# Kernel optimization log

Measured on AMD Instinct MI355X. Metric: run time of the kernel, lower is better.

## Reference

```python
import jax, jax.numpy as jnp
import numpy as np

N_NODES = 40000
N_EDGES = 640000
N_GRAPHS = 64
D_IN = 128
HID = 200
OUT = 2


def _lin(key, fin, fout):
    # torch nn.Linear-style init: U(-1/sqrt(fin), 1/sqrt(fin))
    kw, kb = jax.random.split(key)
    s = 1.0 / np.sqrt(fin)
    W = jax.random.uniform(kw, (fin, fout), jnp.float32, -s, s)
    b = jax.random.uniform(kb, (fout,), jnp.float32, -s, s)
    return W, b


def setup_inputs() -> dict:
    key = jax.random.key(0)
    ks = jax.random.split(key, 10)
    x = jax.random.normal(ks[0], (N_NODES, D_IN), jnp.float32)
    edge_index = jax.random.randint(ks[1], (2, N_EDGES), 0, N_NODES, jnp.int32)
    batch = jnp.sort(jax.random.randint(ks[2], (N_NODES,), 0, N_GRAPHS, jnp.int32))
    W1, b1 = _lin(ks[3], D_IN, HID)
    W2, b2 = _lin(ks[4], HID, HID)
    W3, b3 = _lin(ks[5], HID, HID)
    Wg, bg = _lin(ks[6], HID, HID)
    Wc1, bc1 = _lin(ks[7], HID, HID // 2)
    Wc2, bc2 = _lin(ks[8], HID // 2, OUT)
    return {"x": x, "edge_index": edge_index, "batch": batch,
            "W1": W1, "b1": b1, "W2": W2, "b2": b2, "W3": W3, "b3": b3,
            "Wg": Wg, "bg": bg, "Wc1": Wc1, "bc1": bc1, "Wc2": Wc2, "bc2": bc2}


def reference(x, edge_index, batch, W1, b1, W2, b2, W3, b3, Wg, bg, Wc1, bc1, Wc2, bc2):
    n = x.shape[0]
    # GCNConv with self-loops + symmetric normalization (PyG defaults)
    loop = jnp.arange(n, dtype=edge_index.dtype)
    src = jnp.concatenate([edge_index[0], loop])  # [E+N]
    dst = jnp.concatenate([edge_index[1], loop])
    deg = jax.ops.segment_sum(jnp.ones(src.shape, x.dtype), dst, num_segments=n)
    dinv = jax.lax.rsqrt(jnp.maximum(deg, 1.0))  # deg >= 1 with self-loops
    norm = (dinv[src] * dinv[dst])[:, None]      # [E+N, 1]

    def gcn(h, W, b):
        m = (h @ W)[src] * norm                  # gather + scale per edge
        return jax.ops.segment_sum(m, dst, num_segments=n) + b

    h = jax.nn.relu(gcn(x, W1, b1))
    h = jax.nn.relu(gcn(h, W2, b2))
    h = jax.nn.relu(gcn(h, W3, b3))

    gate = jax.nn.sigmoid(h @ Wg + bg)
    hg = h * gate

    # global_mean_pool over batch assignment
    sums = jax.ops.segment_sum(hg, batch, num_segments=N_GRAPHS)
    cnt = jax.ops.segment_sum(jnp.ones((n,), x.dtype), batch, num_segments=N_GRAPHS)
    pooled = sums / jnp.maximum(cnt, 1.0)[:, None]

    # classifier (dropout is identity in eval)
    hidden = jax.nn.relu(pooled @ Wc1 + bc1)
    logits = hidden @ Wc2 + bc2                  # [N_GRAPHS, 2]
    return logits
```

## Files before the change

### kernel.cpp

```cpp
#include <hip/hip_runtime.h>

#define NG 64
#define HIDW 200
#define DIN 128
#define KPAD 224
#define POOL_NC 8

typedef _Float16 half4_t __attribute__((ext_vector_type(4)));
typedef _Float16 half8_t __attribute__((ext_vector_type(8)));
typedef float floatx4 __attribute__((ext_vector_type(4)));


__global__ void build_kernel(const int* __restrict__ dst, int* __restrict__ counts,
                             const int* __restrict__ batch, int* __restrict__ gs,
                             int E, int n) {
  int i = blockIdx.x * 256 + threadIdx.x;
  if (i < E) atomicAdd(&counts[dst[i]], 1);
  if (i < n) {
    int b = batch[i];
    if (i == 0) {
      for (int g = 0; g <= b; ++g) gs[g] = 0;
    } else {
      int bp = batch[i - 1];
      for (int g = bp + 1; g <= b; ++g) gs[g] = i;
    }
    if (i == n - 1) {
      for (int g = b + 1; g <= NG; ++g) gs[g] = n;
    }
  }
}


__global__ __launch_bounds__(256) void scan1_kernel(const int* __restrict__ counts,
                                                    int* __restrict__ blocksum,
                                                    float* __restrict__ dinv, int n) {
  __shared__ int s[256];
  int tid = threadIdx.x;
  int i = blockIdx.x * 256 + tid;
  int c = (i < n) ? counts[i] : 0;
  if (i < n) dinv[i] = rsqrtf((float)(c + 1));
  s[tid] = c;
  __syncthreads();
#pragma unroll
  for (int off = 128; off > 0; off >>= 1) {
    if (tid < off) s[tid] += s[tid + off];
    __syncthreads();
  }
  if (tid == 0) blocksum[blockIdx.x] = s[0];
}

__global__ __launch_bounds__(1024) void scan2_kernel(int* __restrict__ blocksum, int nb) {
  __shared__ int s[1024];
  int tid = threadIdx.x;
  int v = (tid < nb) ? blocksum[tid] : 0;
  s[tid] = v;
  __syncthreads();
  for (int off = 1; off < 1024; off <<= 1) {
    int t = (tid >= off) ? s[tid - off] : 0;
    __syncthreads();
    s[tid] += t;
    __syncthreads();
  }
  if (tid < nb) blocksum[tid] = s[tid] - v;
}

__global__ __launch_bounds__(256) void scan3_kernel(const int* __restrict__ counts,
                                                    const int* __restrict__ blocksum,
                                                    int* __restrict__ row_ptr, int n) {
  __shared__ int s[256];
  int tid = threadIdx.x;
  int i = blockIdx.x * 256 + tid;
  int c = (i < n) ? counts[i] : 0;
  s[tid] = c;
  __syncthreads();
  for (int off = 1; off < 256; off <<= 1) {
    int t = (tid >= off) ? s[tid - off] : 0;
    __syncthreads();
    s[tid] += t;
    __syncthreads();
  }
  int base = blocksum[blockIdx.x];
  if (i < n) row_ptr[i] = base + s[tid] - c;
  if (i == n - 1) row_ptr[n] = base + s[tid];
}

__global__ void fill_kernel(const int* __restrict__ src, const int* __restrict__ dst,
                            const int* __restrict__ row_ptr, int* __restrict__ fill,
                            int* __restrict__ csr_src, int E) {
  int e = blockIdx.x * 256 + threadIdx.x;
  if (e >= E) return;
  int d = dst[e];
  int pos = row_ptr[d] + atomicAdd(&fill[d], 1);
  csr_src[pos] = src[e];
}


__global__ void wprep_kernel(const float* __restrict__ W1, const float* __restrict__ W2,
                             const float* __restrict__ W3, const float* __restrict__ Wg,
                             _Float16* __restrict__ o1, _Float16* __restrict__ o2,
                             _Float16* __restrict__ o3, _Float16* __restrict__ og) {
  int wsel = blockIdx.y;
  const float* W = (wsel == 0) ? W1 : (wsel == 1) ? W2 : (wsel == 2) ? W3 : Wg;
  _Float16* WT = (wsel == 0) ? o1 : (wsel == 1) ? o2 : (wsel == 2) ? o3 : og;
  int K  = (wsel == 0) ? DIN : HIDW;
  int KP = (wsel == 0) ? DIN : KPAD;
  int idx = blockIdx.x * 256 + threadIdx.x;
  if (idx >= 256 * KP) return;
  int col = idx / KP, k = idx % KP;
  float v = (col < HIDW && k < K) ? W[(long)k * HIDW + col] : 0.f;
  WT[idx] = (_Float16)v;
}


__global__ void cvt_kernel(const float* __restrict__ x, const float* __restrict__ dinv,
                           _Float16* __restrict__ g0, int n) {
  int t = blockIdx.x * 256 + threadIdx.x;
  if (t >= n * 32) return;
  int node = t >> 5, q = t & 31;
  float di = dinv[node];
  float4 v = *(const float4*)&x[(long)node * 128 + q * 4];
  half4_t r = {(_Float16)(di * v.x), (_Float16)(di * v.y),
               (_Float16)(di * v.z), (_Float16)(di * v.w)};
  ((half4_t*)g0)[(long)node * 32 + q] = r;
}


template <int C>
__global__ __launch_bounds__(256) void agg_kernel(const _Float16* __restrict__ g,
                                                  const int* __restrict__ row_ptr,
                                                  const int* __restrict__ csr_src,
                                                  const float* __restrict__ dinv,
                                                  _Float16* __restrict__ out, int n) {
  int node = blockIdx.x * 4 + (threadIdx.x >> 6);
  int lane = threadIdx.x & 63;
  if (node >= n || lane >= C) return;
  const half4_t* __restrict__ hp = (const half4_t*)g;
  int e0 = row_ptr[node], e1 = row_ptr[node + 1];
  half4_t self = hp[(long)node * C + lane];
  float ax = (float)self.x, ay = (float)self.y;
  float az = (float)self.z, aw = (float)self.w;

  int e = e0;
  for (; e + 16 <= e1; e += 16) {
    int sI[16];
#pragma unroll
    for (int j = 0; j < 16; ++j) sI[j] = csr_src[e + j];
    half4_t vv[16];
#pragma unroll
    for (int j = 0; j < 16; ++j) vv[j] = hp[(long)sI[j] * C + lane];
#pragma unroll
    for (int j = 0; j < 16; ++j) {
      ax += (float)vv[j].x; ay += (float)vv[j].y;
      az += (float)vv[j].z; aw += (float)vv[j].w;
    }
  }
  if (e + 8 <= e1) {
    int sI[8];
#pragma unroll
    for (int j = 0; j < 8; ++j) sI[j] = csr_src[e + j];
    half4_t vv[8];
#pragma unroll
    for (int j = 0; j < 8; ++j) vv[j] = hp[(long)sI[j] * C + lane];
#pragma unroll
    for (int j = 0; j < 8; ++j) {
      ax += (float)vv[j].x; ay += (float)vv[j].y;
      az += (float)vv[j].z; aw += (float)vv[j].w;
    }
    e += 8;
  }
  if (e + 4 <= e1) {
    int sI[4];
#pragma unroll
    for (int j = 0; j < 4; ++j) sI[j] = csr_src[e + j];
    half4_t vv[4];
#pragma unroll
    for (int j = 0; j < 4; ++j) vv[j] = hp[(long)sI[j] * C + lane];
#pragma unroll
    for (int j = 0; j < 4; ++j) {
      ax += (float)vv[j].x; ay += (float)vv[j].y;
      az += (float)vv[j].z; aw += (float)vv[j].w;
    }
    e += 4;
  }
  for (; e < e1; ++e) {
    int s = csr_src[e];
    half4_t v = hp[(long)s * C + lane];
    ax += (float)v.x; ay += (float)v.y; az += (float)v.z; aw += (float)v.w;
  }
  float di = dinv[node];
  half4_t r = {(_Float16)(di * ax), (_Float16)(di * ay),
               (_Float16)(di * az), (_Float16)(di * aw)};
  ((half4_t*)out)[(long)node * C + lane] = r;
}


template <int KP, int MODE, int DSCALE>
__global__ __launch_bounds__(256, 2) void mgemm_kernel(const _Float16* __restrict__ A,
                                                       const _Float16* __restrict__ WT,
                                                       const float* __restrict__ bias,
                                                       const float* __restrict__ dinv,
                                                       _Float16* __restrict__ out, int N) {
  constexpr int LDK = KP + 8;
  __shared__ _Float16 Bs[64][LDK];
  int tid = threadIdx.x;
  int b = blockIdx.x;
  int strip = (b >> 3) & 3;
  int rg = (b & 7) + 8 * (b >> 5);
  int col0 = strip * 64;

  {
    int c = tid >> 2;
    int ks = (tid & 3) * (KP / 4);
    const _Float16* gw = WT + (long)(col0 + c) * KP + ks;
#pragma unroll
    for (int j = 0; j < KP / 32; ++j)
      *(half8_t*)&Bs[c][ks + j * 8] = *(const half8_t*)(gw + j * 8);
  }
  __syncthreads();

  int lane = tid & 63;
  int wid = tid >> 6;
  int row0 = rg * 256 + wid * 64;
  if (row0 >= N) return;
  int l15 = lane & 15;
  int lq = lane >> 4;

  const _Float16* __restrict__ pa = A + (long)(row0 + l15) * KP + lq * 8;

  floatx4 acc[4][4];
#pragma unroll
  for (int i = 0; i < 4; ++i)
#pragma unroll
    for (int j = 0; j < 4; ++j) acc[i][j] = (floatx4){0.f, 0.f, 0.f, 0.f};

#pragma unroll
  for (int k0 = 0; k0 < KP; k0 += 32) {
    half8_t a[4];
#pragma unroll
    for (int rf = 0; rf < 4; ++rf)
      a[rf] = *(const half8_t*)(pa + (long)rf * 16 * KP + k0);
#pragma unroll
    for (int cf = 0; cf < 4; ++cf) {
      half8_t bv = *(const half8_t*)&Bs[cf * 16 + l15][k0 + lq * 8];
#pragma unroll
      for (int rf = 0; rf < 4; ++rf)
        acc[rf][cf] = __builtin_amdgcn_mfma_f32_16x16x32_f16(a[rf], bv, acc[rf][cf], 0, 0, 0);
    }
  }

#pragma unroll
  for (int cf = 0; cf < 4; ++cf) {
    int col = col0 + cf * 16 + l15;
    if (col >= KPAD) continue;
    float bs = (col < HIDW) ? bias[col] : 0.f;
#pragma unroll
    for (int rf = 0; rf < 4; ++rf) {
      int rbase = row0 + rf * 16 + lq * 4;
#pragma unroll
      for (int j = 0; j < 4; ++j) {
        int row = rbase + j;
        float v = acc[rf][cf][j] + bs;
        if (MODE == 1) v = fmaxf(v, 0.f);
        if (MODE == 2) {
          float hv = (float)A[(long)row * KP + col];
          v = hv * (1.f / (1.f + __expf(-v)));
        }
        if (DSCALE) v *= dinv[row];
        if (col >= HIDW) v = 0.f;
        out[(long)row * KPAD + col] = (_Float16)v;
      }
    }
  }
}


__global__ __launch_bounds__(256) void pool_partial_kernel(const _Float16* __restrict__ gated,
                                                           const int* __restrict__ gs,
                                                           float* __restrict__ partial, int n) {
  int g = blockIdx.x;
  int c = blockIdx.y;
  int f = threadIdx.x;
  int s = gs[g], e = gs[g + 1];
  int len = e - s;
  int chunk = (len + POOL_NC - 1) / POOL_NC;
  int i0 = s + c * chunk;
  int i1 = i0 + chunk; if (i1 > e) i1 = e;
  if (f < HIDW) {
    float acc = 0.f;
    for (int i = i0; i < i1; ++i) acc += (float)gated[(long)i * KPAD + f];
    partial[(g * POOL_NC + c) * HIDW + f] = acc;
  }
}


__global__ void classifier_kernel(const float* __restrict__ partial,
                                  const int* __restrict__ gs,
                                  const float* __restrict__ Wc1, const float* __restrict__ bc1,
                                  const float* __restrict__ Wc2, const float* __restrict__ bc2,
                                  float* __restrict__ out) {
  int g = blockIdx.x;
  int tid = threadIdx.x;
  __shared__ float pg[HIDW];
  __shared__ float hid[100];
  if (tid < HIDW) {
    float acc = 0.f;
#pragma unroll
    for (int c = 0; c < POOL_NC; ++c) acc += partial[(g * POOL_NC + c) * HIDW + tid];
    float cnt = fmaxf((float)(gs[g + 1] - gs[g]), 1.f);
    pg[tid] = acc / cnt;
  }
  __syncthreads();
  if (tid < 100) {
    float a = bc1[tid];
    for (int k = 0; k < HIDW; ++k) a = fmaf(pg[k], Wc1[k * 100 + tid], a);
    hid[tid] = fmaxf(a, 0.f);
  }
  __syncthreads();
  if (tid < 2) {
    float a = bc2[tid];
    for (int k = 0; k < 100; ++k) a = fmaf(hid[k], Wc2[k * 2 + tid], a);
    out[g * 2 + tid] = a;
  }
}


extern "C" void kernel_launch(void* const* d_in, const int* in_sizes, int n_in,
                              void* d_out, int out_size, void* d_ws, size_t ws_size,
                              hipStream_t stream) {
  const float* x    = (const float*)d_in[0];
  const int*   ei   = (const int*)d_in[1];
  const int*   batch= (const int*)d_in[2];
  const float* W1 = (const float*)d_in[3];  const float* b1 = (const float*)d_in[4];
  const float* W2 = (const float*)d_in[5];  const float* b2 = (const float*)d_in[6];
  const float* W3 = (const float*)d_in[7];  const float* b3 = (const float*)d_in[8];
  const float* Wg = (const float*)d_in[9];  const float* bg = (const float*)d_in[10];
  const float* Wc1= (const float*)d_in[11]; const float* bc1= (const float*)d_in[12];
  const float* Wc2= (const float*)d_in[13]; const float* bc2= (const float*)d_in[14];
  float* out = (float*)d_out;

  const int n = in_sizes[0] / DIN;
  const int E = in_sizes[1] / 2;
  const int* src = ei;
  const int* dst = ei + E;
  const int nb256 = (n + 255) / 256;

  int* counts   = (int*)d_ws;
  int* fill     = counts + n;
  int* row_ptr  = fill + n;
  int* gs       = row_ptr + (n + 4);
  int* blocksum = gs + 68;
  float* dinv   = (float*)(blocksum + 1024);
  int* csr_src  = (int*)(dinv + n);
  float* partial= (float*)(csr_src + E);
  _Float16* wt1 = (_Float16*)(partial + NG * POOL_NC * HIDW);
  _Float16* wt2 = wt1 + 256 * 128;
  _Float16* wt3 = wt2 + 256 * KPAD;
  _Float16* wtg = wt3 + 256 * KPAD;
  _Float16* xh   = wtg + 256 * KPAD;
  _Float16* bufA = xh + (long)n * DIN;
  _Float16* bufB = bufA + (long)n * KPAD;

  hipMemsetAsync(counts, 0, (size_t)2 * n * sizeof(int), stream);

  dim3 wgrid((256 * KPAD + 255) / 256, 4);
  wprep_kernel<<<wgrid, 256, 0, stream>>>(W1, W2, W3, Wg, wt1, wt2, wt3, wtg);

  int eb = (E + 255) / 256;
  build_kernel<<<eb, 256, 0, stream>>>(dst, counts, batch, gs, E, n);
  scan1_kernel<<<nb256, 256, 0, stream>>>(counts, blocksum, dinv, n);
  cvt_kernel<<<(n * 32 + 255) / 256, 256, 0, stream>>>(x, dinv, xh, n);
  scan2_kernel<<<1, 1024, 0, stream>>>(blocksum, nb256);
  scan3_kernel<<<nb256, 256, 0, stream>>>(counts, blocksum, row_ptr, n);
  fill_kernel<<<eb, 256, 0, stream>>>(src, dst, row_ptr, fill, csr_src, E);

  int ab = (n + 3) / 4;
  int gb = ((nb256 + 7) / 8) * 8 * 4;

  agg_kernel<32><<<ab, 256, 0, stream>>>(xh, row_ptr, csr_src, dinv, bufA, n);
  mgemm_kernel<DIN, 1, 1><<<gb, 256, 0, stream>>>(bufA, wt1, b1, dinv, bufB, n);
  agg_kernel<56><<<ab, 256, 0, stream>>>(bufB, row_ptr, csr_src, dinv, bufA, n);
  mgemm_kernel<KPAD, 1, 1><<<gb, 256, 0, stream>>>(bufA, wt2, b2, dinv, bufB, n);
  agg_kernel<56><<<ab, 256, 0, stream>>>(bufB, row_ptr, csr_src, dinv, bufA, n);
  mgemm_kernel<KPAD, 1, 0><<<gb, 256, 0, stream>>>(bufA, wt3, b3, dinv, bufB, n);
  mgemm_kernel<KPAD, 2, 0><<<gb, 256, 0, stream>>>(bufB, wtg, bg, dinv, bufA, n);
  dim3 pgrid(NG, POOL_NC);
  pool_partial_kernel<<<pgrid, 256, 0, stream>>>(bufA, gs, partial, n);
  classifier_kernel<<<NG, 256, 0, stream>>>(partial, gs, Wc1, bc1, Wc2, bc2, out);
}
```

Baseline: 319.3 us.

## Shrink activation row stride to 200, halve GEMM row tile, fold scan2 into scan3

Activation buffers now use a row stride of 200 halfs instead of the padded 224, so the aggregation kernels move about 11% fewer bytes per gather. The GEMM keeps 224-wide K for the weights but reads A with stride 200. Reads past column 200 land in the next row, or in a 64-element pad at the end of the buffer, and meet zero-padded weight rows, so they add nothing. The GEMM tile drops from 256 to 128 rows per block with launch bounds raised to 4, giving more blocks and occupancy. The single-block scan2 is removed: each scan3 block reduces the earlier block sums itself, saving one launch at the cost of redundant reductions.

```diff
diff --git a/kernel.cpp b/kernel.cpp
--- a/kernel.cpp
+++ b/kernel.cpp
@@ -3,7 +3,7 @@
 #define NG 64
 #define HIDW 200
 #define DIN 128
-#define KPAD 224
+#define WKP 224
 #define POOL_NC 8
 
 typedef _Float16 half4_t __attribute__((ext_vector_type(4)));
@@ -49,26 +49,22 @@
   if (tid == 0) blocksum[blockIdx.x] = s[0];
 }
 
-__global__ __launch_bounds__(1024) void scan2_kernel(int* __restrict__ blocksum, int nb) {
-  __shared__ int s[1024];
-  int tid = threadIdx.x;
-  int v = (tid < nb) ? blocksum[tid] : 0;
-  s[tid] = v;
-  __syncthreads();
-  for (int off = 1; off < 1024; off <<= 1) {
-    int t = (tid >= off) ? s[tid - off] : 0;
-    __syncthreads();
-    s[tid] += t;
-    __syncthreads();
-  }
-  if (tid < nb) blocksum[tid] = s[tid] - v;
-}
 
 __global__ __launch_bounds__(256) void scan3_kernel(const int* __restrict__ counts,
                                                     const int* __restrict__ blocksum,
-                                                    int* __restrict__ row_ptr, int n) {
+                                                    int* __restrict__ row_ptr, int n, int nb) {
+  __shared__ int bs[256];
   __shared__ int s[256];
   int tid = threadIdx.x;
+  bs[tid] = (tid < blockIdx.x && tid < nb) ? blocksum[tid] : 0;
+  __syncthreads();
+#pragma unroll
+  for (int off = 128; off > 0; off >>= 1) {
+    if (tid < off) bs[tid] += bs[tid + off];
+    __syncthreads();
+  }
+  int base = bs[0];
+
   int i = blockIdx.x * 256 + tid;
   int c = (i < n) ? counts[i] : 0;
   s[tid] = c;
@@ -79,7 +75,6 @@
     s[tid] += t;
     __syncthreads();
   }
-  int base = blocksum[blockIdx.x];
   if (i < n) row_ptr[i] = base + s[tid] - c;
   if (i == n - 1) row_ptr[n] = base + s[tid];
 }
@@ -103,7 +98,7 @@
   const float* W = (wsel == 0) ? W1 : (wsel == 1) ? W2 : (wsel == 2) ? W3 : Wg;
   _Float16* WT = (wsel == 0) ? o1 : (wsel == 1) ? o2 : (wsel == 2) ? o3 : og;
   int K  = (wsel == 0) ? DIN : HIDW;
-  int KP = (wsel == 0) ? DIN : KPAD;
+  int KP = (wsel == 0) ? DIN : WKP;
   int idx = blockIdx.x * 256 + threadIdx.x;
   if (idx >= 256 * KP) return;
   int col = idx / KP, k = idx % KP;
@@ -194,8 +189,8 @@
 }
 
 
-template <int KP, int MODE, int DSCALE>
-__global__ __launch_bounds__(256, 2) void mgemm_kernel(const _Float16* __restrict__ A,
+template <int KP, int AS, int MODE, int DSCALE>
+__global__ __launch_bounds__(256, 4) void mgemm_kernel(const _Float16* __restrict__ A,
                                                        const _Float16* __restrict__ WT,
                                                        const float* __restrict__ bias,
                                                        const float* __restrict__ dinv,
@@ -220,30 +215,30 @@
 
   int lane = tid & 63;
   int wid = tid >> 6;
-  int row0 = rg * 256 + wid * 64;
+  int row0 = rg * 128 + wid * 32;
   if (row0 >= N) return;
   int l15 = lane & 15;
   int lq = lane >> 4;
 
-  const _Float16* __restrict__ pa = A + (long)(row0 + l15) * KP + lq * 8;
-
-  floatx4 acc[4][4];
-#pragma unroll
-  for (int i = 0; i < 4; ++i)
+  const _Float16* __restrict__ pa = A + (long)(row0 + l15) * AS + lq * 8;
+
+  floatx4 acc[2][4];
+#pragma unroll
+  for (int i = 0; i < 2; ++i)
 #pragma unroll
     for (int j = 0; j < 4; ++j) acc[i][j] = (floatx4){0.f, 0.f, 0.f, 0.f};
 
 #pragma unroll
   for (int k0 = 0; k0 < KP; k0 += 32) {
-    half8_t a[4];
-#pragma unroll
-    for (int rf = 0; rf < 4; ++rf)
-      a[rf] = *(const half8_t*)(pa + (long)rf * 16 * KP + k0);
+    half8_t a[2];
+#pragma unroll
+    for (int rf = 0; rf < 2; ++rf)
+      a[rf] = *(const half8_t*)(pa + (long)rf * 16 * AS + k0);
 #pragma unroll
     for (int cf = 0; cf < 4; ++cf) {
       half8_t bv = *(const half8_t*)&Bs[cf * 16 + l15][k0 + lq * 8];
 #pragma unroll
-      for (int rf = 0; rf < 4; ++rf)
+      for (int rf = 0; rf < 2; ++rf)
         acc[rf][cf] = __builtin_amdgcn_mfma_f32_16x16x32_f16(a[rf], bv, acc[rf][cf], 0, 0, 0);
     }
   }
@@ -251,10 +246,10 @@
 #pragma unroll
   for (int cf = 0; cf < 4; ++cf) {
     int col = col0 + cf * 16 + l15;
-    if (col >= KPAD) continue;
-    float bs = (col < HIDW) ? bias[col] : 0.f;
-#pragma unroll
-    for (int rf = 0; rf < 4; ++rf) {
+    if (col >= HIDW) continue;
+    float bs = bias[col];
+#pragma unroll
+    for (int rf = 0; rf < 2; ++rf) {
       int rbase = row0 + rf * 16 + lq * 4;
 #pragma unroll
       for (int j = 0; j < 4; ++j) {
@@ -262,12 +257,11 @@
         float v = acc[rf][cf][j] + bs;
         if (MODE == 1) v = fmaxf(v, 0.f);
         if (MODE == 2) {
-          float hv = (float)A[(long)row * KP + col];
+          float hv = (float)A[(long)row * AS + col];
           v = hv * (1.f / (1.f + __expf(-v)));
         }
         if (DSCALE) v *= dinv[row];
-        if (col >= HIDW) v = 0.f;
-        out[(long)row * KPAD + col] = (_Float16)v;
+        out[(long)row * HIDW + col] = (_Float16)v;
       }
     }
   }
@@ -287,7 +281,7 @@
   int i1 = i0 + chunk; if (i1 > e) i1 = e;
   if (f < HIDW) {
     float acc = 0.f;
-    for (int i = i0; i < i1; ++i) acc += (float)gated[(long)i * KPAD + f];
+    for (int i = i0; i < i1; ++i) acc += (float)gated[(long)i * HIDW + f];
     partial[(g * POOL_NC + c) * HIDW + f] = acc;
   }
 }
@@ -353,36 +347,36 @@
   int* csr_src  = (int*)(dinv + n);
   float* partial= (float*)(csr_src + E);
   _Float16* wt1 = (_Float16*)(partial + NG * POOL_NC * HIDW);
-  _Float16* wt2 = wt1 + 256 * 128;
-  _Float16* wt3 = wt2 + 256 * KPAD;
-  _Float16* wtg = wt3 + 256 * KPAD;
-  _Float16* xh   = wtg + 256 * KPAD;
+  _Float16* wt2 = wt1 + 256 * DIN;
+  _Float16* wt3 = wt2 + 256 * WKP;
+  _Float16* wtg = wt3 + 256 * WKP;
+  _Float16* xh   = wtg + 256 * WKP;
   _Float16* bufA = xh + (long)n * DIN;
-  _Float16* bufB = bufA + (long)n * KPAD;
+  _Float16* bufB = bufA + (long)n * HIDW + 64;
 
   hipMemsetAsync(counts, 0, (size_t)2 * n * sizeof(int), stream);
 
-  dim3 wgrid((256 * KPAD + 255) / 256, 4);
+  dim3 wgrid((256 * WKP + 255) / 256, 4);
   wprep_kernel<<<wgrid, 256, 0, stream>>>(W1, W2, W3, Wg, wt1, wt2, wt3, wtg);
 
   int eb = (E + 255) / 256;
   build_kernel<<<eb, 256, 0, stream>>>(dst, counts, batch, gs, E, n);
   scan1_kernel<<<nb256, 256, 0, stream>>>(counts, blocksum, dinv, n);
   cvt_kernel<<<(n * 32 + 255) / 256, 256, 0, stream>>>(x, dinv, xh, n);
-  scan2_kernel<<<1, 1024, 0, stream>>>(blocksum, nb256);
-  scan3_kernel<<<nb256, 256, 0, stream>>>(counts, blocksum, row_ptr, n);
+  scan3_kernel<<<nb256, 256, 0, stream>>>(counts, blocksum, row_ptr, n, nb256);
   fill_kernel<<<eb, 256, 0, stream>>>(src, dst, row_ptr, fill, csr_src, E);
 
   int ab = (n + 3) / 4;
-  int gb = ((nb256 + 7) / 8) * 8 * 4;
+  int nrg = (n + 127) / 128;
+  int gb = ((nrg + 7) / 8) * 8 * 4;
 
   agg_kernel<32><<<ab, 256, 0, stream>>>(xh, row_ptr, csr_src, dinv, bufA, n);
-  mgemm_kernel<DIN, 1, 1><<<gb, 256, 0, stream>>>(bufA, wt1, b1, dinv, bufB, n);
-  agg_kernel<56><<<ab, 256, 0, stream>>>(bufB, row_ptr, csr_src, dinv, bufA, n);
-  mgemm_kernel<KPAD, 1, 1><<<gb, 256, 0, stream>>>(bufA, wt2, b2, dinv, bufB, n);
-  agg_kernel<56><<<ab, 256, 0, stream>>>(bufB, row_ptr, csr_src, dinv, bufA, n);
-  mgemm_kernel<KPAD, 1, 0><<<gb, 256, 0, stream>>>(bufA, wt3, b3, dinv, bufB, n);
-  mgemm_kernel<KPAD, 2, 0><<<gb, 256, 0, stream>>>(bufB, wtg, bg, dinv, bufA, n);
+  mgemm_kernel<DIN, DIN, 1, 1><<<gb, 256, 0, stream>>>(bufA, wt1, b1, dinv, bufB, n);
+  agg_kernel<50><<<ab, 256, 0, stream>>>(bufB, row_ptr, csr_src, dinv, bufA, n);
+  mgemm_kernel<WKP, HIDW, 1, 1><<<gb, 256, 0, stream>>>(bufA, wt2, b2, dinv, bufB, n);
+  agg_kernel<50><<<ab, 256, 0, stream>>>(bufB, row_ptr, csr_src, dinv, bufA, n);
+  mgemm_kernel<WKP, HIDW, 1, 0><<<gb, 256, 0, stream>>>(bufA, wt3, b3, dinv, bufB, n);
+  mgemm_kernel<WKP, HIDW, 2, 0><<<gb, 256, 0, stream>>>(bufB, wtg, bg, dinv, bufA, n);
   dim3 pgrid(NG, POOL_NC);
   pool_partial_kernel<<<pgrid, 256, 0, stream>>>(bufA, gs, partial, n);
   classifier_kernel<<<NG, 256, 0, stream>>>(partial, gs, Wc1, bc1, Wc2, bc2, out);
```

Measured after the change: 301.3 us (median of 2 runs). -5.6%, faster.
